# Kernel optimization log

Measured on AMD Instinct MI355X. Metric: run time of the kernel, lower is better.

Reference implementation:

```python
import jax, jax.numpy as jnp
import numpy as np

B, S, D = 8, 8192, 1024
FILTER_SIZE = 4


def setup_inputs() -> dict:
    key = jax.random.key(0)
    k1, k2, k3 = jax.random.split(key, 3)
    x = jax.random.normal(k1, (B, S, D), dtype=jnp.float32)
    # projection to [bias, filter_size coefficients]
    W = jax.random.normal(k2, (D, FILTER_SIZE + 1), dtype=jnp.float32) / np.sqrt(D)
    noise = jax.random.uniform(k3, (B, S, 1), dtype=jnp.float32)
    return {"x": x, "W": W, "noise": noise}


def reference(x, W, noise):
    """Sequentially-dependent gater.
    gate_logits[i] = log p(g_i=1 | g_{<i}), gate_probs[i] = p, gate_samples[i] ~ Bernoulli(p).
    Filter weights are a linear projection of x; the per-step logit is
    bias + <coeffs, last filter_size samples> (zeros before t=0).
    Returns (gate_logits, gate_probs, gate_samples), each [B, S, 1].
    """
    b, s, d = x.shape
    fsz = W.shape[1] - 1
    # precompute_filter_weights: [B, S, 1+filter_size]
    fw = jnp.einsum('bsd,df->bsf', x, W)

    def step(window, inputs):
        # window: [B, fsz] most recent samples, oldest first
        fw_t, u_t = inputs  # [B, 1+fsz], [B]
        logit = fw_t[:, 0] + jnp.sum(window * fw_t[:, 1:], axis=-1)  # [B]
        logp = jax.nn.log_sigmoid(logit)
        p = jax.nn.sigmoid(logit)
        samp = (u_t < p).astype(x.dtype)
        new_window = jnp.concatenate([window[:, 1:], samp[:, None]], axis=1)
        return new_window, (logp, p, samp)

    window0 = jnp.zeros((b, fsz), dtype=x.dtype)
    xs = (jnp.swapaxes(fw, 0, 1), jnp.swapaxes(noise[..., 0], 0, 1))  # [S, B, ...]
    _, (logps, ps, samps) = jax.lax.scan(step, window0, xs)

    to_out = lambda a: jnp.swapaxes(a, 0, 1)[..., None]  # [S,B] -> [B,S,1]
    return to_out(logps), to_out(ps), to_out(samps)
```

## Files before the change

### kernel.cpp

```cpp
#include <hip/hip_runtime.h>
#include <cstdint>
#include <cstddef>


namespace {

constexpr int kB = 8;
constexpr int kS = 8192;
constexpr int kD = 1024;
constexpr int kRows = kB * kS;
constexpr int kT = 64;
constexpr int kCPB = kS / kT;
constexpr int kChunks = kB * kCPB;
constexpr unsigned long long kIdMap = 0xFEDCBA9876543210ull;

__device__ __forceinline__ float logit_from_state(unsigned int w,
                                                  const float4& A,
                                                  const float4& Bv) {
  const float s1 = (w & 1u) ? A.y : 0.0f;
  const float s2 = (w & 2u) ? A.z : 0.0f;
  const float s3 = (w & 4u) ? A.w : 0.0f;
  const float s4 = (w & 8u) ? Bv.x : 0.0f;
  return A.x + (((s1 + s2) + s3) + s4);
}

__device__ __forceinline__ unsigned long long compose(unsigned long long a,
                                                      unsigned long long b) {
  unsigned long long r = 0;
#pragma unroll
  for (int s = 0; s < 16; ++s) {
    const unsigned int e = (unsigned int)(a >> (4 * s)) & 15u;
    r |= ((b >> (4 * e)) & 15ull) << (4 * s);
  }
  return r;
}

}

__global__ __launch_bounds__(256, 4) void proj_map_kernel(
    const float* __restrict__ x, const float* __restrict__ W,
    const float* __restrict__ noise, float* __restrict__ fwu,
    unsigned long long* __restrict__ trajbuf,
    unsigned long long* __restrict__ maps) {
  __shared__ float Wl[kD * 5];
  __shared__ float fl[kT * 8];
  const int tid = threadIdx.x;

  const float4* W4 = reinterpret_cast<const float4*>(W);
  float4* Wl4 = reinterpret_cast<float4*>(Wl);
#pragma unroll
  for (int i = 0; i < 5; ++i) Wl4[tid + 256 * i] = W4[tid + 256 * i];
  __syncthreads();

  const int lane = tid & 63;
  const int wv = tid >> 6;
  const int chunk = blockIdx.x;
  const int r0 = chunk * kT;

  float wr[4][4][5];
#pragma unroll
  for (int j = 0; j < 4; ++j)
#pragma unroll
    for (int k = 0; k < 4; ++k) {
      const int d = j * 256 + lane * 4 + k;
#pragma unroll
      for (int f = 0; f < 5; ++f) wr[j][k][f] = Wl[d * 5 + f];
    }

#pragma unroll 1
  for (int t = 0; t < 16; ++t) {
    const int rl = wv * 16 + t;
    const int row = r0 + rl;
    const float4* xr = reinterpret_cast<const float4*>(x + (size_t)row * kD);
    float acc[5] = {0.f, 0.f, 0.f, 0.f, 0.f};
#pragma unroll
    for (int j = 0; j < 4; ++j) {
      const float4 v = xr[j * 64 + lane];
      const float e[4] = {v.x, v.y, v.z, v.w};
#pragma unroll
      for (int k = 0; k < 4; ++k)
#pragma unroll
        for (int f = 0; f < 5; ++f) acc[f] += e[k] * wr[j][k][f];
    }
#pragma unroll
    for (int off = 32; off >= 1; off >>= 1)
#pragma unroll
      for (int f = 0; f < 5; ++f) acc[f] += __shfl_xor(acc[f], off);

    if (lane == 0) {
      const float u = noise[row];
      const float th = logf(u / (1.0f - u));
      const float4 o0 = make_float4(acc[0], acc[1], acc[2], acc[3]);
      const float4 o1 = make_float4(acc[4], u, th, 0.0f);
      float4* og = reinterpret_cast<float4*>(fwu + (size_t)row * 8);
      og[0] = o0;
      og[1] = o1;
      float4* ol = reinterpret_cast<float4*>(&fl[rl * 8]);
      ol[0] = o0;
      ol[1] = o1;
    }
  }
  __syncthreads();

  if (wv == 0) {
    unsigned int cur = (unsigned int)(lane & 15);
    unsigned long long traj = 0;
#pragma unroll 8
    for (int i = 0; i < kT; ++i) {
      const float4* p = reinterpret_cast<const float4*>(&fl[i * 8]);
      const float4 A = p[0];
      const float4 Bv = p[1];
      const unsigned int d = (logit_from_state(cur, A, Bv) > Bv.z) ? 1u : 0u;
      traj |= (unsigned long long)d << i;
      cur = (cur >> 1) | (d << 3);
    }
    if (lane < 16) trajbuf[(size_t)chunk * 16 + lane] = traj;
    const unsigned long long b0 = __ballot((int)(cur & 1u));
    const unsigned long long b1 = __ballot((int)(cur & 2u));
    const unsigned long long b2 = __ballot((int)(cur & 4u));
    const unsigned long long b3 = __ballot((int)(cur & 8u));
    if (lane == 0) {
      unsigned long long m = 0;
#pragma unroll
      for (int s = 0; s < 16; ++s) {
        const unsigned long long e =
            ((b0 >> s) & 1ull) | (((b1 >> s) & 1ull) << 1) |
            (((b2 >> s) & 1ull) << 2) | (((b3 >> s) & 1ull) << 3);
        m |= e << (4 * s);
      }
      maps[chunk] = m;
    }
  }
}

__global__ __launch_bounds__(256) void scan_emit_kernel(
    const float* __restrict__ fwu, const unsigned long long* __restrict__ maps,
    const unsigned long long* __restrict__ trajbuf, float* __restrict__ out) {
  __shared__ unsigned int starts_lds[kCPB];
  const int tid = threadIdx.x;
  const int lane = tid & 63;
  const int wv = tid >> 6;
  const int c0 = blockIdx.x * 4;
  const int b = c0 / kCPB;

  if (wv == 0) {
    const int L = lane;
    const unsigned long long m0 = maps[b * kCPB + 2 * L];
    const unsigned long long m1 = maps[b * kCPB + 2 * L + 1];
    unsigned long long scan = compose(m0, m1);
#pragma unroll
    for (int off = 1; off < 64; off <<= 1) {
      const unsigned long long prev = __shfl_up(scan, off);
      if (L >= off) scan = compose(prev, scan);
    }
    unsigned long long pref = __shfl_up(scan, 1);
    if (L == 0) pref = kIdMap;
    const unsigned int s0 = (unsigned int)(pref & 15ull);
    starts_lds[2 * L] = s0;
    starts_lds[2 * L + 1] = (unsigned int)((m0 >> (4 * s0)) & 15ull);
  }
  __syncthreads();

  const int chunk = c0 + wv;
  const unsigned int st = starts_lds[chunk & (kCPB - 1)];
  const unsigned long long traj = trajbuf[(size_t)chunk * 16 + st];
  const int row = chunk * kT + lane;

  const float4* p = reinterpret_cast<const float4*>(fwu + (size_t)row * 8);
  const float4 A = p[0];
  const float4 Bv = p[1];

  unsigned int w;
  if (lane >= 4)
    w = (unsigned int)(traj >> (lane - 4)) & 15u;
  else
    w = ((st >> lane) | ((unsigned int)traj << (4 - lane))) & 15u;

  const float logit = logit_from_state(w, A, Bv);
  const float pr = 1.0f / (1.0f + expf(-logit));
  const float lp = fminf(logit, 0.0f) - log1pf(expf(-fabsf(logit)));
  out[row] = lp;
  out[kRows + row] = pr;
  out[2 * kRows + row] = (float)((traj >> lane) & 1ull);
}

extern "C" void kernel_launch(void* const* d_in, const int* in_sizes, int n_in,
                              void* d_out, int out_size, void* d_ws,
                              size_t ws_size, hipStream_t stream) {
  const float* x = (const float*)d_in[0];
  const float* W = (const float*)d_in[1];
  const float* noise = (const float*)d_in[2];
  float* out = (float*)d_out;

  float* fwu = (float*)d_ws;
  unsigned long long* trajbuf =
      (unsigned long long*)((char*)d_ws + (size_t)kRows * 8 * sizeof(float));
  unsigned long long* maps =
      (unsigned long long*)((char*)trajbuf +
                            (size_t)kChunks * 16 * sizeof(unsigned long long));

  proj_map_kernel<<<kChunks, 256, 0, stream>>>(x, W, noise, fwu, trajbuf, maps);
  scan_emit_kernel<<<kChunks / 4, 256, 0, stream>>>(fwu, maps, trajbuf, out);
}
```

Before: 60.35 us.

## Double-buffer x row loads and hoist noise/trajectory loads ahead of sync

In the projection kernel, each wave now prefetches the next x rows into two register buffers while it computes the current row. Occupancy is relaxed to 2 blocks per SM to leave room for the extra registers. Noise values and their logit thresholds are loaded once per wave and passed to each row with shuffles. In the scan kernel, the fwu and trajectory loads are issued before the prefix-scan barrier, and the right trajectory is picked with a shuffle, so load latency overlaps the scan. The cost is higher register pressure and lower occupancy in the memory-bound projection kernel.

Measured after the change: 60.85 us. No clear change (+0.8%).

```diff
diff --git a/kernel.cpp b/kernel.cpp
--- a/kernel.cpp
+++ b/kernel.cpp
@@ -37,7 +37,7 @@
 
 }
 
-__global__ __launch_bounds__(256, 4) void proj_map_kernel(
+__global__ __launch_bounds__(256, 2) void proj_map_kernel(
     const float* __restrict__ x, const float* __restrict__ W,
     const float* __restrict__ noise, float* __restrict__ fwu,
     unsigned long long* __restrict__ trajbuf,
@@ -56,6 +56,7 @@
   const int wv = tid >> 6;
   const int chunk = blockIdx.x;
   const int r0 = chunk * kT;
+  const int rw0 = r0 + wv * 16;
 
   float wr[4][4][5];
 #pragma unroll
@@ -67,16 +68,26 @@
       for (int f = 0; f < 5; ++f) wr[j][k][f] = Wl[d * 5 + f];
     }
 
-#pragma unroll 1
-  for (int t = 0; t < 16; ++t) {
-    const int rl = wv * 16 + t;
-    const int row = r0 + rl;
-    const float4* xr = reinterpret_cast<const float4*>(x + (size_t)row * kD);
+  float nu = 0.5f, nth = 0.0f;
+  if (lane < 16) {
+    nu = noise[rw0 + lane];
+    nth = logf(nu / (1.0f - nu));
+  }
+
+  auto pref = [&](float4(&v)[4], int t) {
+    if (t < 16) {
+      const float4* xp =
+          reinterpret_cast<const float4*>(x + (size_t)(rw0 + t) * kD);
+#pragma unroll
+      for (int j = 0; j < 4; ++j) v[j] = xp[j * 64 + lane];
+    }
+  };
+
+  auto do_row = [&](const float4(&v)[4], int t) {
     float acc[5] = {0.f, 0.f, 0.f, 0.f, 0.f};
 #pragma unroll
     for (int j = 0; j < 4; ++j) {
-      const float4 v = xr[j * 64 + lane];
-      const float e[4] = {v.x, v.y, v.z, v.w};
+      const float e[4] = {v[j].x, v[j].y, v[j].z, v[j].w};
 #pragma unroll
       for (int k = 0; k < 4; ++k)
 #pragma unroll
@@ -87,18 +98,30 @@
 #pragma unroll
       for (int f = 0; f < 5; ++f) acc[f] += __shfl_xor(acc[f], off);
 
+    const float u = __shfl(nu, t);
+    const float th = __shfl(nth, t);
     if (lane == 0) {
-      const float u = noise[row];
-      const float th = logf(u / (1.0f - u));
+      const int row = rw0 + t;
       const float4 o0 = make_float4(acc[0], acc[1], acc[2], acc[3]);
       const float4 o1 = make_float4(acc[4], u, th, 0.0f);
       float4* og = reinterpret_cast<float4*>(fwu + (size_t)row * 8);
       og[0] = o0;
       og[1] = o1;
-      float4* ol = reinterpret_cast<float4*>(&fl[rl * 8]);
+      float4* ol = reinterpret_cast<float4*>(&fl[(wv * 16 + t) * 8]);
       ol[0] = o0;
       ol[1] = o1;
     }
+  };
+
+  float4 va[4], vb[4];
+  pref(va, 0);
+  pref(vb, 1);
+#pragma unroll 1
+  for (int tp = 0; tp < 8; ++tp) {
+    do_row(va, 2 * tp);
+    pref(va, 2 * tp + 2);
+    do_row(vb, 2 * tp + 1);
+    pref(vb, 2 * tp + 3);
   }
   __syncthreads();
 
@@ -142,6 +165,14 @@
   const int wv = tid >> 6;
   const int c0 = blockIdx.x * 4;
   const int b = c0 / kCPB;
+  const int chunk = c0 + wv;
+  const int row = chunk * kT + lane;
+
+  const float4* p = reinterpret_cast<const float4*>(fwu + (size_t)row * 8);
+  const float4 A = p[0];
+  const float4 Bv = p[1];
+  unsigned long long tj = 0;
+  if (lane < 16) tj = trajbuf[(size_t)chunk * 16 + lane];
 
   if (wv == 0) {
     const int L = lane;
@@ -161,14 +192,8 @@
   }
   __syncthreads();
 
-  const int chunk = c0 + wv;
   const unsigned int st = starts_lds[chunk & (kCPB - 1)];
-  const unsigned long long traj = trajbuf[(size_t)chunk * 16 + st];
-  const int row = chunk * kT + lane;
-
-  const float4* p = reinterpret_cast<const float4*>(fwu + (size_t)row * 8);
-  const float4 A = p[0];
-  const float4 Bv = p[1];
+  const unsigned long long traj = __shfl(tj, (int)st);
 
   unsigned int w;
   if (lane >= 4)
```
